# Optimization experiments

Hardware: AMD Instinct MI355X
Metric: run time of the kernel (lower is better)

## Reference

```python
import jax, jax.numpy as jnp
import numpy as np

B, P, M = 2, 2048, 1024
H, D = 16, 64  # num_heads, head_dim; M == H*D

def setup_inputs() -> dict:
    key = jax.random.key(0)
    k1, k2, k3 = jax.random.split(key, 3)
    x = jax.random.normal(k1, (B, P, M), dtype=jnp.float32)
    W_attn = jax.random.normal(k2, (M, 3 * M), dtype=jnp.float32) * 0.02
    b_attn = jnp.zeros((3 * M,), dtype=jnp.float32)
    W_proj = jax.random.normal(k3, (M, M), dtype=jnp.float32) * 0.02
    b_proj = jnp.zeros((M,), dtype=jnp.float32)
    return {"x": x, "W_attn": W_attn, "b_attn": b_attn, "W_proj": W_proj, "b_proj": b_proj}

def reference(x, W_attn, b_attn, W_proj, b_proj):
    b, p, m = x.shape
    # fused QKV projection
    qkv = jnp.einsum('bpm,mn->bpn', x, W_attn) + b_attn  # [b,p,3m]
    q, k, v = jnp.split(qkv, 3, axis=2)
    q = q.reshape(b, p, H, D)
    k = k.reshape(b, p, H, D)
    v = v.reshape(b, p, H, D)
    q = q / jnp.sqrt(jnp.asarray(D, dtype=q.dtype))
    scores = jnp.einsum('bqhd,bkhd->bhqk', q, k)  # [b,h,p,p]
    causal = jnp.tril(jnp.ones((p, p), dtype=bool))  # [p,p]
    big_neg = jnp.finfo(jnp.float32).min
    scores = jnp.where(causal[None, None, :, :], scores, big_neg)
    pattern = jax.nn.softmax(scores, axis=-1)
    z = jnp.einsum('bhqk,bkhd->bqhd', pattern, v)  # [b,p,h,d]
    z = z.reshape(b, p, m)
    out = jnp.einsum('bpm,mn->bpn', z, W_proj) + b_proj
    return out
```

## Files before the change

kernel.cpp:

```cpp
#include <hip/hip_runtime.h>
#include <hip/hip_bf16.h>

typedef __bf16 bf16;
typedef __attribute__((ext_vector_type(8))) __bf16 bf16x8;
typedef __attribute__((ext_vector_type(4))) float f32x4;

#define MFMA16(a, b, c) __builtin_amdgcn_mfma_f32_16x16x32_bf16(a, b, c, 0, 0, 0)
#define GLL16(gp, lp)                                                          \
  __builtin_amdgcn_global_load_lds(                                            \
      (const __attribute__((address_space(1))) void*)(gp),                     \
      (__attribute__((address_space(3))) void*)(lp), 16, 0, 0)

constexpr int Bsz = 2, Pseq = 2048, Mdim = 1024, NH = 16, Dh = 64;
constexpr int ROWS = Bsz * Pseq;
constexpr float LOG2E = 1.4426950408889634f;
constexpr float BIG_NEG = -3.0e38f;
constexpr float M0 = 8.0f;

__global__ void k_cvt(const float* __restrict__ X, bf16* __restrict__ Xb, int n4) {
  int i = blockIdx.x * blockDim.x + threadIdx.x;
  int stride = gridDim.x * blockDim.x;
  const f32x4* X4 = (const f32x4*)X;
  for (; i < n4; i += stride) {
    f32x4 v = X4[i];
    union { bf16 h[4]; uint2 u; } pk;
    pk.h[0] = (bf16)v[0]; pk.h[1] = (bf16)v[1];
    pk.h[2] = (bf16)v[2]; pk.h[3] = (bf16)v[3];
    ((uint2*)Xb)[i] = pk.u;
  }
}

__global__ void k_transpose_cvt(const float* __restrict__ W, bf16* __restrict__ Wt,
                                int Ndim, int Kdim) {
  __shared__ __align__(16) bf16 tile[64][72];
  int n0 = blockIdx.x * 64, k0 = blockIdx.y * 64;
  int t = threadIdx.x;
  int tc = t & 15, tr = t >> 4;
#pragma unroll
  for (int pass = 0; pass < 4; ++pass) {
    int r = tr + pass * 16;
    f32x4 v = *(const f32x4*)(W + (size_t)(k0 + r) * Ndim + n0 + tc * 4);
#pragma unroll
    for (int i = 0; i < 4; ++i) tile[tc * 4 + i][r] = (bf16)v[i];
  }
  __syncthreads();
#pragma unroll
  for (int pass = 0; pass < 4; ++pass) {
    int n = tr + pass * 16;
    union { bf16 h[4]; uint2 u; } pk;
#pragma unroll
    for (int i = 0; i < 4; ++i) pk.h[i] = tile[n][tc * 4 + i];
    *(uint2*)(Wt + (size_t)(n0 + n) * Kdim + k0 + tc * 4) = pk.u;
  }
}

template <int TN>
__device__ __forceinline__ void gemm_core(const bf16* __restrict__ A,
                                          const bf16* __restrict__ Bt,
                                          bf16* Ash, bf16* Bsh, int K,
                                          int row0, int col0,
                                          f32x4 (&acc)[4][TN / 32]) {
  constexpr int NT = TN / 32;
  int tid = threadIdx.x;
  int lane = tid & 63, w = tid >> 6;
  int l15 = lane & 15, g = lane >> 4, l7 = lane & 7, l8 = lane >> 3;
  int wm = w & 1, wn = w >> 1;
  const bf16* Ag = A + (size_t)(row0 + w * 8 + l8) * K + (l7 ^ l8) * 8;
  const bf16* Bg = Bt + (size_t)(col0 + w * 8 + l8) * K + (l7 ^ l8) * 8;
  bf16* Asb = Ash + w * 512;
  bf16* Bsb = Bsh + w * 512;
  for (int k0 = 0; k0 < K; k0 += 64) {
#pragma unroll
    for (int p = 0; p < 4; ++p)
      GLL16(Ag + (size_t)(p * 32) * K + k0, Asb + p * 2048);
#pragma unroll
    for (int p = 0; p < NT; ++p)
      GLL16(Bg + (size_t)(p * 32) * K + k0, Bsb + p * 2048);
    __syncthreads();
#pragma unroll
    for (int ks = 0; ks < 2; ++ks) {
      int swz = ((ks * 4 + g) ^ l7) * 8;
      bf16x8 af[4], bfr[NT];
#pragma unroll
      for (int mt = 0; mt < 4; ++mt)
        af[mt] = *(const bf16x8*)(Ash + (wm * 64 + mt * 16 + l15) * 64 + swz);
#pragma unroll
      for (int nt = 0; nt < NT; ++nt)
        bfr[nt] = *(const bf16x8*)(Bsh + (wn * (TN / 2) + nt * 16 + l15) * 64 + swz);
#pragma unroll
      for (int mt = 0; mt < 4; ++mt)
#pragma unroll
        for (int nt = 0; nt < NT; ++nt)
          acc[mt][nt] = MFMA16(af[mt], bfr[nt], acc[mt][nt]);
    }
    __syncthreads();
  }
}

__global__ __launch_bounds__(256) void k_qkv(const bf16* __restrict__ Xb,
                                             const bf16* __restrict__ Wt,
                                             const float* __restrict__ bias,
                                             bf16* __restrict__ Qo,
                                             bf16* __restrict__ Ko,
                                             bf16* __restrict__ Vto) {
  __shared__ __align__(16) bf16 Ash[128 * 64], Bsh[128 * 64];
  int cb = blockIdx.x, rb = blockIdx.y;
  int row0 = rb * 128, col0 = cb * 128;
  f32x4 acc[4][4];
  const f32x4 zero = {0.f, 0.f, 0.f, 0.f};
#pragma unroll
  for (int mt = 0; mt < 4; ++mt)
#pragma unroll
    for (int nt = 0; nt < 4; ++nt) acc[mt][nt] = zero;
  gemm_core<128>(Xb, Wt, Ash, Bsh, Mdim, row0, col0, acc);

  int lane = threadIdx.x & 63, w = threadIdx.x >> 6;
  int l15 = lane & 15, g = lane >> 4;
  int wm = w & 1, wn = w >> 1;
  int sec = cb >> 3;
  if (sec < 2) {
    bf16* out = sec == 0 ? Qo : Ko;
    float scale = sec == 0 ? (0.125f * LOG2E) : 1.0f;
#pragma unroll
    for (int nt = 0; nt < 4; ++nt) {
      int col = col0 + wn * 64 + nt * 16 + l15;
      int cm = col & 1023;
      int h = cm >> 6, d = cm & 63;
      float bv = bias[col];
#pragma unroll
      for (int mt = 0; mt < 4; ++mt)
#pragma unroll
        for (int r = 0; r < 4; ++r) {
          int row = row0 + wm * 64 + mt * 16 + g * 4 + r;
          int b = row >> 11, p = row & 2047;
          out[(size_t)((b * NH + h) * Pseq + p) * Dh + d] =
              (bf16)((acc[mt][nt][r] + bv) * scale);
        }
    }
  } else {
#pragma unroll
    for (int nt = 0; nt < 4; ++nt) {
      int col = col0 + wn * 64 + nt * 16 + l15;
      int cm = col & 1023;
      int h = cm >> 6, d = cm & 63;
      float bv = bias[col];
#pragma unroll
      for (int mt = 0; mt < 4; ++mt) {
        int row = row0 + wm * 64 + mt * 16 + g * 4;
        int b = row >> 11, p = row & 2047;
        union { bf16 hh[4]; uint2 u; } pk;
#pragma unroll
        for (int r = 0; r < 4; ++r) pk.hh[r] = (bf16)(acc[mt][nt][r] + bv);
        *(uint2*)(Vto + ((size_t)((b * NH + h) * Dh + d)) * Pseq + p) = pk.u;
      }
    }
  }
}

__global__ __launch_bounds__(256, 4) void k_attn(const bf16* __restrict__ Q,
                                                 const bf16* __restrict__ K,
                                                 const bf16* __restrict__ Vt,
                                                 bf16* __restrict__ Z) {
  __shared__ __align__(16) bf16 Ksh[2 * 64 * 64];
  __shared__ __align__(16) bf16 Vsh[2 * 64 * 64];
  __shared__ __align__(16) bf16 Pb[4 * 16 * 64];
  int bh = blockIdx.x;
  int y = blockIdx.y;
  int qt = (y < 16) ? y : 47 - y;
  int b = bh >> 4, h = bh & 15;
  const bf16* Qb = Q + (size_t)bh * Pseq * Dh;
  const bf16* Kb = K + (size_t)bh * Pseq * Dh;
  const bf16* Vb = Vt + (size_t)bh * Dh * Pseq;
  int tid = threadIdx.x;
  int lane = tid & 63, w = tid >> 6;
  int l15 = lane & 15, g = lane >> 4, l7 = lane & 7;
  int q0 = qt * 64;
  int njt = qt + 1;

  bf16x8 qf[2];
#pragma unroll
  for (int ks = 0; ks < 2; ++ks)
    qf[ks] = *(const bf16x8*)(Qb + (size_t)(q0 + w * 16 + l15) * Dh + ks * 32 + g * 8);

  f32x4 O[4];
  const f32x4 zero = {0.f, 0.f, 0.f, 0.f};
#pragma unroll
  for (int nt = 0; nt < 4; ++nt) O[nt] = zero;
  float lacc[4] = {0.f, 0.f, 0.f, 0.f};

  int srow = tid >> 3;
  int sgr = (tid & 7) ^ (srow & 7);
  const bf16* Kgs = Kb + (size_t)srow * Dh + sgr * 8;
  const bf16* Vgs = Vb + (size_t)srow * Pseq + sgr * 8;
  bf16* Pw = Pb + w * 1024;
  int pwr[4], prd[2];
#pragma unroll
  for (int mtl = 0; mtl < 4; ++mtl)
    pwr[mtl] = l15 * 64 + (((mtl * 2 + (g >> 1)) ^ l7) * 8) + (g & 1) * 4;
#pragma unroll
  for (int kl = 0; kl < 2; ++kl)
    prd[kl] = l15 * 64 + (((kl * 4 + g) ^ l7) * 8);

#pragma unroll
  for (int p = 0; p < 2; ++p) {
    GLL16(Kgs + (size_t)(p * 32) * Dh, Ksh + p * 2048 + tid * 8);
    GLL16(Vgs + (size_t)(p * 32) * Pseq, Vsh + p * 2048 + tid * 8);
  }

  for (int j = 0; j < njt; ++j) {
    int buf = j & 1;
    __syncthreads();
    if (j + 1 < njt) {
      const bf16* Kg2 = Kgs + (size_t)((j + 1) * 64) * Dh;
      const bf16* Vg2 = Vgs + (j + 1) * 64;
      bf16* kd = Ksh + (buf ^ 1) * 4096 + tid * 8;
      bf16* vd = Vsh + (buf ^ 1) * 4096 + tid * 8;
#pragma unroll
      for (int p = 0; p < 2; ++p) {
        GLL16(Kg2 + (size_t)(p * 32) * Dh, kd + p * 2048);
        GLL16(Vg2 + (size_t)(p * 32) * Pseq, vd + p * 2048);
      }
    }
    f32x4 S[4];
#pragma unroll
    for (int mt = 0; mt < 4; ++mt) S[mt] = zero;
    const bf16* Kr = Ksh + buf * 4096;
    const bf16* Vr = Vsh + buf * 4096;
#pragma unroll
    for (int ks = 0; ks < 2; ++ks) {
      int swz = ((ks * 4 + g) ^ l7) * 8;
#pragma unroll
      for (int mt = 0; mt < 4; ++mt) {
        bf16x8 kf = *(const bf16x8*)(Kr + (mt * 16 + l15) * 64 + swz);
        S[mt] = MFMA16(kf, qf[ks], S[mt]);
      }
    }
    if (j == njt - 1) {
      int q = q0 + w * 16 + l15;
#pragma unroll
      for (int mt = 0; mt < 4; ++mt) {
        int kvb = j * 64 + mt * 16 + g * 4;
#pragma unroll
        for (int r = 0; r < 4; ++r)
          if (kvb + r > q) S[mt][r] = BIG_NEG;
      }
    }
#pragma unroll
    for (int mt = 0; mt < 4; ++mt) {
      union { bf16 hh[4]; uint2 u; } pk;
#pragma unroll
      for (int r = 0; r < 4; ++r) {
        float p = __builtin_amdgcn_exp2f(S[mt][r] - M0);
        lacc[r] += p;
        pk.hh[r] = (bf16)p;
      }
      *(uint2*)(Pw + pwr[mt]) = pk.u;
    }
#pragma unroll
    for (int kl = 0; kl < 2; ++kl) {
      bf16x8 pf = *(const bf16x8*)(Pw + prd[kl]);
      int swz = ((kl * 4 + g) ^ l7) * 8;
#pragma unroll
      for (int nt = 0; nt < 4; ++nt) {
        bf16x8 vf = *(const bf16x8*)(Vr + (nt * 16 + l15) * 64 + swz);
        O[nt] = MFMA16(pf, vf, O[nt]);
      }
    }
  }
  float l_i = (lacc[0] + lacc[1]) + (lacc[2] + lacc[3]);
  l_i += __shfl_xor(l_i, 16);
  l_i += __shfl_xor(l_i, 32);
#pragma unroll
  for (int r = 0; r < 4; ++r) {
    float li = __shfl(l_i, g * 4 + r);
    float inv = 1.0f / li;
    int q = q0 + w * 16 + g * 4 + r;
    size_t base = ((size_t)(b * Pseq + q)) * Mdim + h * Dh;
#pragma unroll
    for (int nt = 0; nt < 4; ++nt)
      Z[base + nt * 16 + l15] = (bf16)(O[nt][r] * inv);
  }
}

__global__ __launch_bounds__(256) void k_proj(const bf16* __restrict__ Zb,
                                              const bf16* __restrict__ Wt,
                                              const float* __restrict__ bias,
                                              float* __restrict__ Out) {
  __shared__ __align__(16) bf16 Ash[128 * 64], Bsh[64 * 64];
  int cb = blockIdx.x, rb = blockIdx.y;
  int row0 = rb * 128, col0 = cb * 64;
  f32x4 acc[4][2];
  const f32x4 zero = {0.f, 0.f, 0.f, 0.f};
#pragma unroll
  for (int mt = 0; mt < 4; ++mt)
#pragma unroll
    for (int nt = 0; nt < 2; ++nt) acc[mt][nt] = zero;
  gemm_core<64>(Zb, Wt, Ash, Bsh, Mdim, row0, col0, acc);

  int lane = threadIdx.x & 63, w = threadIdx.x >> 6;
  int l15 = lane & 15, g = lane >> 4;
  int wm = w & 1, wn = w >> 1;
#pragma unroll
  for (int nt = 0; nt < 2; ++nt) {
    int col = col0 + wn * 32 + nt * 16 + l15;
    float bv = bias[col];
#pragma unroll
    for (int mt = 0; mt < 4; ++mt)
#pragma unroll
      for (int r = 0; r < 4; ++r) {
        int row = row0 + wm * 64 + mt * 16 + g * 4 + r;
        Out[(size_t)row * Mdim + col] = acc[mt][nt][r] + bv;
      }
  }
}

extern "C" void kernel_launch(void* const* d_in, const int* in_sizes, int n_in,
                              void* d_out, int out_size, void* d_ws, size_t ws_size,
                              hipStream_t stream) {
  const float* x = (const float*)d_in[0];
  const float* W_attn = (const float*)d_in[1];
  const float* b_attn = (const float*)d_in[2];
  const float* W_proj = (const float*)d_in[3];
  const float* b_proj = (const float*)d_in[4];
  float* out = (float*)d_out;

  bf16* Xb = (bf16*)d_ws;
  bf16* Wat = Xb + (size_t)ROWS * Mdim;
  bf16* Wpt = Wat + (size_t)3 * Mdim * Mdim;
  bf16* Qs = Wpt + (size_t)Mdim * Mdim;
  bf16* Ks = Qs + (size_t)ROWS * Mdim;
  bf16* Vts = Ks + (size_t)ROWS * Mdim;
  bf16* Zb = Vts + (size_t)ROWS * Mdim;

  k_cvt<<<1024, 256, 0, stream>>>(x, Xb, ROWS * Mdim / 4);
  k_transpose_cvt<<<dim3(3 * Mdim / 64, Mdim / 64), 256, 0, stream>>>(W_attn, Wat, 3 * Mdim, Mdim);
  k_transpose_cvt<<<dim3(Mdim / 64, Mdim / 64), 256, 0, stream>>>(W_proj, Wpt, Mdim, Mdim);
  k_qkv<<<dim3(3 * Mdim / 128, ROWS / 128), 256, 0, stream>>>(Xb, Wat, b_attn, Qs, Ks, Vts);
  k_attn<<<dim3(Bsz * NH, Pseq / 64), 256, 0, stream>>>(Qs, Ks, Vts, Zb);
  k_proj<<<dim3(Mdim / 64, ROWS / 128), 256, 0, stream>>>(Zb, Wpt, b_proj, out);
}
```

Baseline: 180.4 us.

## Merge preprocessing kernels into one launch and shrink GEMM K-tile to 32

Folds the x conversion and both weight transpose-conversions into a single k_pre launch, dispatching on block index, so two kernel launches and their tails go away. Separately, the shared GEMM core now stages 32-wide K slices instead of 64, with a new XOR swizzle and one 16-byte global-to-LDS load per thread per operand half. This halves LDS use per block and may allow more resident blocks, but it doubles the number of barrier pairs per K loop and gives each sync less MFMA work to hide load latency.

Result: slower. 185.3 us (+2.7%).

```diff
diff --git a/kernel.cpp b/kernel.cpp
--- a/kernel.cpp
+++ b/kernel.cpp
@@ -17,24 +17,39 @@
 constexpr float BIG_NEG = -3.0e38f;
 constexpr float M0 = 8.0f;
 
-__global__ void k_cvt(const float* __restrict__ X, bf16* __restrict__ Xb, int n4) {
-  int i = blockIdx.x * blockDim.x + threadIdx.x;
-  int stride = gridDim.x * blockDim.x;
-  const f32x4* X4 = (const f32x4*)X;
-  for (; i < n4; i += stride) {
-    f32x4 v = X4[i];
-    union { bf16 h[4]; uint2 u; } pk;
-    pk.h[0] = (bf16)v[0]; pk.h[1] = (bf16)v[1];
-    pk.h[2] = (bf16)v[2]; pk.h[3] = (bf16)v[3];
-    ((uint2*)Xb)[i] = pk.u;
-  }
-}
-
-__global__ void k_transpose_cvt(const float* __restrict__ W, bf16* __restrict__ Wt,
-                                int Ndim, int Kdim) {
+__global__ __launch_bounds__(256) void k_pre(const float* __restrict__ X,
+                                             bf16* __restrict__ Xb,
+                                             const float* __restrict__ Wa,
+                                             bf16* __restrict__ Wat,
+                                             const float* __restrict__ Wp,
+                                             bf16* __restrict__ Wpt) {
   __shared__ __align__(16) bf16 tile[64][72];
-  int n0 = blockIdx.x * 64, k0 = blockIdx.y * 64;
+  int blk = blockIdx.x;
   int t = threadIdx.x;
+  if (blk < 1024) {
+    const f32x4* X4 = (const f32x4*)X;
+    int i0 = blk * 1024 + t;
+#pragma unroll
+    for (int c = 0; c < 4; ++c) {
+      int i = i0 + c * 256;
+      f32x4 v = X4[i];
+      union { bf16 h[4]; uint2 u; } pk;
+      pk.h[0] = (bf16)v[0]; pk.h[1] = (bf16)v[1];
+      pk.h[2] = (bf16)v[2]; pk.h[3] = (bf16)v[3];
+      ((uint2*)Xb)[i] = pk.u;
+    }
+    return;
+  }
+  const float* W; bf16* Wt; int Ndim, n0, k0;
+  if (blk < 1792) {
+    int bx = blk - 1024;
+    W = Wa; Wt = Wat; Ndim = 3 * Mdim;
+    n0 = (bx % 48) * 64; k0 = (bx / 48) * 64;
+  } else {
+    int bx = blk - 1792;
+    W = Wp; Wt = Wpt; Ndim = Mdim;
+    n0 = (bx & 15) * 64; k0 = (bx >> 4) * 64;
+  }
   int tc = t & 15, tr = t >> 4;
 #pragma unroll
   for (int pass = 0; pass < 4; ++pass) {
@@ -50,7 +65,7 @@
     union { bf16 h[4]; uint2 u; } pk;
 #pragma unroll
     for (int i = 0; i < 4; ++i) pk.h[i] = tile[n][tc * 4 + i];
-    *(uint2*)(Wt + (size_t)(n0 + n) * Kdim + k0 + tc * 4) = pk.u;
+    *(uint2*)(Wt + (size_t)(n0 + n) * Mdim + k0 + tc * 4) = pk.u;
   }
 }
 
@@ -63,36 +78,31 @@
   constexpr int NT = TN / 32;
   int tid = threadIdx.x;
   int lane = tid & 63, w = tid >> 6;
-  int l15 = lane & 15, g = lane >> 4, l7 = lane & 7, l8 = lane >> 3;
+  int l15 = lane & 15, g = lane >> 4;
   int wm = w & 1, wn = w >> 1;
-  const bf16* Ag = A + (size_t)(row0 + w * 8 + l8) * K + (l7 ^ l8) * 8;
-  const bf16* Bg = Bt + (size_t)(col0 + w * 8 + l8) * K + (l7 ^ l8) * 8;
-  bf16* Asb = Ash + w * 512;
-  bf16* Bsb = Bsh + w * 512;
-  for (int k0 = 0; k0 < K; k0 += 64) {
-#pragma unroll
-    for (int p = 0; p < 4; ++p)
-      GLL16(Ag + (size_t)(p * 32) * K + k0, Asb + p * 2048);
-#pragma unroll
-    for (int p = 0; p < NT; ++p)
-      GLL16(Bg + (size_t)(p * 32) * K + k0, Bsb + p * 2048);
+  int sr = tid >> 2;
+  int sc = (tid & 3) ^ ((sr >> 1) & 3);
+  const bf16* Ag = A + (size_t)(row0 + sr) * K + sc * 8;
+  const bf16* Bg = Bt + (size_t)(col0 + sr) * K + sc * 8;
+  int pg = (l15 >> 1) & 3;
+  for (int k0 = 0; k0 < K; k0 += 32) {
+    GLL16(Ag + k0, Ash + tid * 8);
+    GLL16(Ag + (size_t)64 * K + k0, Ash + 2048 + tid * 8);
+    GLL16(Bg + k0, Bsh + tid * 8);
+    if (NT == 4) GLL16(Bg + (size_t)64 * K + k0, Bsh + 2048 + tid * 8);
     __syncthreads();
-#pragma unroll
-    for (int ks = 0; ks < 2; ++ks) {
-      int swz = ((ks * 4 + g) ^ l7) * 8;
-      bf16x8 af[4], bfr[NT];
-#pragma unroll
-      for (int mt = 0; mt < 4; ++mt)
-        af[mt] = *(const bf16x8*)(Ash + (wm * 64 + mt * 16 + l15) * 64 + swz);
+    bf16x8 af[4], bfr[NT];
+#pragma unroll
+    for (int mt = 0; mt < 4; ++mt)
+      af[mt] = *(const bf16x8*)(Ash + (wm * 64 + mt * 16 + l15) * 32 + (g ^ pg) * 8);
+#pragma unroll
+    for (int nt = 0; nt < NT; ++nt)
+      bfr[nt] = *(const bf16x8*)(Bsh + (wn * (TN / 2) + nt * 16 + l15) * 32 + (g ^ pg) * 8);
+#pragma unroll
+    for (int mt = 0; mt < 4; ++mt)
 #pragma unroll
       for (int nt = 0; nt < NT; ++nt)
-        bfr[nt] = *(const bf16x8*)(Bsh + (wn * (TN / 2) + nt * 16 + l15) * 64 + swz);
-#pragma unroll
-      for (int mt = 0; mt < 4; ++mt)
-#pragma unroll
-        for (int nt = 0; nt < NT; ++nt)
-          acc[mt][nt] = MFMA16(af[mt], bfr[nt], acc[mt][nt]);
-    }
+        acc[mt][nt] = MFMA16(af[mt], bfr[nt], acc[mt][nt]);
     __syncthreads();
   }
 }
@@ -103,7 +113,7 @@
                                              bf16* __restrict__ Qo,
                                              bf16* __restrict__ Ko,
                                              bf16* __restrict__ Vto) {
-  __shared__ __align__(16) bf16 Ash[128 * 64], Bsh[128 * 64];
+  __shared__ __align__(16) bf16 Ash[128 * 32], Bsh[128 * 32];
   int cb = blockIdx.x, rb = blockIdx.y;
   int row0 = rb * 128, col0 = cb * 128;
   f32x4 acc[4][4];
@@ -286,7 +296,7 @@
                                               const bf16* __restrict__ Wt,
                                               const float* __restrict__ bias,
                                               float* __restrict__ Out) {
-  __shared__ __align__(16) bf16 Ash[128 * 64], Bsh[64 * 64];
+  __shared__ __align__(16) bf16 Ash[128 * 32], Bsh[64 * 32];
   int cb = blockIdx.x, rb = blockIdx.y;
   int row0 = rb * 128, col0 = cb * 64;
   f32x4 acc[4][2];
@@ -332,9 +342,7 @@
   bf16* Vts = Ks + (size_t)ROWS * Mdim;
   bf16* Zb = Vts + (size_t)ROWS * Mdim;
 
-  k_cvt<<<1024, 256, 0, stream>>>(x, Xb, ROWS * Mdim / 4);
-  k_transpose_cvt<<<dim3(3 * Mdim / 64, Mdim / 64), 256, 0, stream>>>(W_attn, Wat, 3 * Mdim, Mdim);
-  k_transpose_cvt<<<dim3(Mdim / 64, Mdim / 64), 256, 0, stream>>>(W_proj, Wpt, Mdim, Mdim);
+  k_pre<<<2048, 256, 0, stream>>>(x, Xb, W_attn, Wat, W_proj, Wpt);
   k_qkv<<<dim3(3 * Mdim / 128, ROWS / 128), 256, 0, stream>>>(Xb, Wat, b_attn, Qs, Ks, Vts);
   k_attn<<<dim3(Bsz * NH, Pseq / 64), 256, 0, stream>>>(Qs, Ks, Vts, Zb);
   k_proj<<<dim3(Mdim / 64, ROWS / 128), 256, 0, stream>>>(Zb, Wpt, b_proj, out);
```
